# Kernel tuning notes

Measured on AMD Instinct MI355X. Metric: run time of the kernel, lower is better.

The kernel has to match this reference:

```python
import jax, jax.numpy as jnp
import numpy as np

N_NODES = 50000
IN_CH = 128
N_EDGES = 800000
ADD_CONST = 0.5


def setup_inputs() -> dict:
    key = jax.random.key(0)
    k1, k2, k3, k4, k5 = jax.random.split(key, 5)
    x = jax.random.normal(k1, (N_NODES, IN_CH), dtype=jnp.float32)
    edge_index = jax.random.randint(k2, (2, N_EDGES), 0, N_NODES, dtype=jnp.int32)
    edge_weight = jax.random.uniform(k3, (N_EDGES,), dtype=jnp.float32)
    # Linear(2*C -> 1): split into source/target halves (mathematically identical
    # to Linear on concat([x[row], x[col]])). Xavier-uniform-ish scale.
    lim = float(np.sqrt(6.0 / (2 * IN_CH + 1)))
    w_src = jax.random.uniform(k4, (IN_CH,), minval=-lim, maxval=lim, dtype=jnp.float32)
    w_dst = jax.random.uniform(k5, (IN_CH,), minval=-lim, maxval=lim, dtype=jnp.float32)
    b = jnp.zeros((), dtype=jnp.float32)
    return {"x": x, "w_src": w_src, "w_dst": w_dst, "b": b,
            "edge_index": edge_index, "edge_weight": edge_weight}


def _normalize_edge_score(score, row, num_nodes):
    """Per-source-node softmax over strictly-positive scores, +0.5; nodes with
    no positive incident edge keep raw scores (faithful to torch loop)."""
    pos = score > 0
    has_pos = jax.ops.segment_max(pos.astype(jnp.int32), row, num_segments=num_nodes) > 0
    neg_big = jnp.asarray(jnp.finfo(score.dtype).min, score.dtype)
    smax = jax.ops.segment_max(jnp.where(pos, score, neg_big), row, num_segments=num_nodes)
    safe_max = jnp.where(has_pos, smax, 0.0)
    exp_s = jnp.where(pos, jnp.exp(score - safe_max[row]), 0.0)
    denom = jax.ops.segment_sum(exp_s, row, num_segments=num_nodes)
    denom = jnp.where(denom > 0, denom, 1.0)
    soft = jnp.where(pos, exp_s / denom[row] + ADD_CONST, 0.0)
    return jnp.where(has_pos[row], soft, score)


def reference(x, w_src, w_dst, b, edge_index, edge_weight):
    N = x.shape[0]
    row, col = edge_index[0], edge_index[1]

    # Edge score: Linear on concat([x[row], x[col]]) == per-node projections gathered.
    score = (x @ w_src)[row] + (x @ w_dst)[col] + b          # [E]
    norm = _normalize_edge_score(score, row, N)              # [E]

    # Greedy contraction in descending score order. Because the torch loop skips
    # any edge whose endpoint cluster already has size > 1, this is exactly a
    # greedy maximal matching: carry only a per-node 'matched' bitmask.
    perm = jnp.argsort(-norm)
    r_s, c_s, s_s = row[perm], col[perm], norm[perm]

    def step(matched, uv):
        u, v = uv
        ok = (u != v) & ~matched[u] & ~matched[v]
        matched = matched.at[u].set(matched[u] | ok)
        matched = matched.at[v].set(matched[v] | ok)
        return matched, ok

    _, sel = jax.lax.scan(step, jnp.zeros((N,), dtype=bool), (r_s, c_s))  # sel: [E]

    # cluster[v] = u for each selected edge (u, v); everything else identity.
    drop_v = jnp.where(sel, c_s, N)   # out-of-range indices are dropped
    drop_u = jnp.where(sel, r_s, N)
    cluster = jnp.arange(N, dtype=jnp.int32).at[drop_v].set(r_s, mode='drop')
    s_rep = jnp.ones((N,), x.dtype).at[drop_u].set(s_s, mode='drop')       # score of merging edge at rep u
    partner = jnp.arange(N, dtype=jnp.int32).at[drop_u].set(c_s, mode='drop')
    rep_sel = jnp.zeros((N,), bool).at[drop_u].set(True, mode='drop')

    # torch: merged_x[u] = (x[u] + x[v]) * s ; merged_x[v] stays x[v];
    # new_x = index_add by cluster  =>  rep u gets (x[u]+x[v])*s + x[v].
    sum_x = jax.ops.segment_sum(x, cluster, num_segments=N)               # [N, C]
    new_x = sum_x * s_rep[:, None] + jnp.where(rep_sel[:, None], x[partner], 0.0)

    counts = jax.ops.segment_sum(jnp.ones((N,), jnp.int32), cluster, num_segments=N)
    is_rep = counts > 0          # rows of new_x that correspond to surviving clusters

    # Remap edges to cluster representatives; self-loops masked out.
    new_row = cluster[row]
    new_col = cluster[col]
    edge_valid = new_row != new_col

    return new_x, cluster, is_rep, new_row, new_col, edge_valid, edge_weight
```

## Files before the change

### kernel.cpp

```cpp
#include <hip/hip_runtime.h>
#include <cmath>

#define IN_CH 128
#define NBUCK 256
#define LNMAX 196
#define SIDE_BIT (1u << 20)
#define SELF_BIT (1u << 21)
#define PLW(p) __hip_atomic_load((p), __ATOMIC_RELAXED, __HIP_MEMORY_SCOPE_WORKGROUP)

typedef unsigned long long ull;
typedef ull  ull2 __attribute__((ext_vector_type(2)));
typedef float f4  __attribute__((ext_vector_type(4)));

__device__ __forceinline__ ull make_key(float norm, int e) {
    unsigned int b = __float_as_uint(norm);
    unsigned int asc = (b & 0x80000000u) ? ~b : (b | 0x80000000u);
    unsigned int desc = ~asc;
    return (((ull)desc) << 32) | (unsigned int)e;
}

__device__ __forceinline__ float norm_from(float s, unsigned int mb, double den) {
    if (mb != 0u) {
        if (s > 0.0f) {
            float m = __uint_as_float(mb);
            float ev = (float)exp((double)(s - m));
            float d = (float)den;
            return ev / d + 0.5f;
        }
        return 0.0f;
    }
    return s;
}

__global__ void proj_kernel(const float* __restrict__ x, const float* __restrict__ w_src,
                            const float* __restrict__ w_dst, float* __restrict__ p,
                            float* __restrict__ q,
                            ull* __restrict__ wsuit,
                            int* __restrict__ cluster, int* __restrict__ partner,
                            float* __restrict__ s_rep, int* __restrict__ bump,
                            int* __restrict__ btail, int N) {
    int gtid = blockIdx.x * blockDim.x + threadIdx.x;
    if (gtid == 0) *bump = 0;
    if (gtid < NBUCK) btail[gtid] = 0;
    if (gtid < N) {
        wsuit[gtid]    = ~0ULL;
        cluster[gtid]  = gtid;
        partner[gtid]  = gtid;
        s_rep[gtid]    = 1.0f;
    }
    int wave = gtid >> 6;
    int lane = threadIdx.x & 63;
    if (wave >= N) return;
    float2 xv = ((const float2*)(x + (size_t)wave * IN_CH))[lane];
    float2 ws = ((const float2*)w_src)[lane];
    float2 wd = ((const float2*)w_dst)[lane];
    double ap = (double)xv.x * (double)ws.x + (double)xv.y * (double)ws.y;
    double aq = (double)xv.x * (double)wd.x + (double)xv.y * (double)wd.y;
    #pragma unroll
    for (int off = 32; off > 0; off >>= 1) {
        ap += __shfl_down(ap, off);
        aq += __shfl_down(aq, off);
    }
    if (lane == 0) { p[wave] = (float)ap; q[wave] = (float)aq; }
}

__global__ void score_kernel(const int* __restrict__ row, const int* __restrict__ col,
                             const float* __restrict__ p, const float* __restrict__ q,
                             const float* __restrict__ bptr,
                             int2* __restrict__ rc, int* __restrict__ btail,
                             uint2* __restrict__ bucketA, float* __restrict__ bucketS,
                             int bcap, int E) {
    __shared__ int cnt[NBUCK];
    __shared__ int gbase[NBUCK];
    __shared__ int cincl[NBUCK];
    __shared__ unsigned int sA0[2048];
    __shared__ unsigned int sA1[2048];
    __shared__ float sS[2048];
    __shared__ unsigned short sH[2048];
    int t = threadIdx.x;
    int e = blockIdx.x * blockDim.x + t;
    if (t < NBUCK) cnt[t] = 0;
    __syncthreads();
    bool inb = e < E;
    int u = 0, v = 0, l1 = -1, l2 = -1, h1 = 0, h2 = 0;
    float s = 0.0f;
    if (inb) {
        u = row[e]; v = col[e];
        rc[e] = make_int2(u, v);
        s = p[u] + q[v] + bptr[0];
        h1 = u & (NBUCK - 1); l1 = atomicAdd(&cnt[h1], 1);
        if (u != v) {
            h2 = v & (NBUCK - 1); l2 = atomicAdd(&cnt[h2], 1);
        }
    }
    __syncthreads();
    if (t < NBUCK) cincl[t] = cnt[t];
    __syncthreads();
    #pragma unroll
    for (int off = 1; off < NBUCK; off <<= 1) {
        int add = (t < NBUCK && t >= off) ? cincl[t - off] : 0;
        __syncthreads();
        if (t < NBUCK) cincl[t] += add;
        __syncthreads();
    }
    if (t < NBUCK) gbase[t] = atomicAdd(&btail[t], cnt[t]);
    __syncthreads();
    int total = cincl[NBUCK - 1];
    if (l1 >= 0) {
        int idx = cincl[h1] - cnt[h1] + l1;
        sA0[idx] = (unsigned int)e | ((u == v) ? SELF_BIT : 0u);
        sA1[idx] = (unsigned int)v | ((unsigned int)(u >> 8) << 17);
        sS[idx]  = s;
        sH[idx]  = (unsigned short)h1;
    }
    if (l2 >= 0) {
        int idx = cincl[h2] - cnt[h2] + l2;
        sA0[idx] = (unsigned int)e | SIDE_BIT;
        sA1[idx] = (unsigned int)u | ((unsigned int)(v >> 8) << 17);
        sS[idx]  = s;
        sH[idx]  = (unsigned short)h2;
    }
    __syncthreads();
    for (int i = t; i < total; i += blockDim.x) {
        int h = (int)sH[i];
        int pos = gbase[h] + (i - (cincl[h] - cnt[h]));
        size_t g = (size_t)h * bcap + pos;
        bucketA[g] = make_uint2(sA0[i], sA1[i]);
        bucketS[g] = sS[i];
    }
}

__global__ void slot_kernel(uint2* __restrict__ bucketA, const float* __restrict__ bucketS,
                            const int* __restrict__ btail, int bcap,
                            unsigned int* __restrict__ node_max, double* __restrict__ denom,
                            int* __restrict__ bump, int2* __restrict__ seg, int N) {
    __shared__ int hist[LNMAX];
    __shared__ unsigned int maxv[LNMAX];
    __shared__ double dden[LNMAX];
    __shared__ int scan[256];
    __shared__ int basesh;
    int b = blockIdx.x;
    int t = threadIdx.x;
    for (int i = t; i < LNMAX; i += blockDim.x) {
        hist[i] = 0; maxv[i] = 0u; dden[i] = 0.0;
    }
    __syncthreads();
    int n = btail[b];
    uint2* bkA = bucketA + (size_t)b * bcap;
    const float* bkS = bucketS + (size_t)b * bcap;
    for (int i = t; i < n; i += blockDim.x) {
        uint2 en = bkA[i];
        if (!(en.x & SIDE_BIT)) {
            float s = bkS[i];
            if (s > 0.0f) {
                int ln = (int)((en.y >> 17) & 0x1ffu);
                atomicMax(&maxv[ln], __float_as_uint(s));
            }
        }
    }
    __syncthreads();
    for (int i = t; i < n; i += blockDim.x) {
        uint2 en = bkA[i];
        int ln = (int)((en.y >> 17) & 0x1ffu);
        if (!(en.x & SIDE_BIT)) {
            unsigned int mb = maxv[ln];
            float s = bkS[i];
            if (mb != 0u && s > 0.0f) {
                float m = __uint_as_float(mb);
                float ev = (float)exp((double)(s - m));
                atomicAdd(&dden[ln], (double)ev);
            }
        }
        if (en.x & SELF_BIT) {
            bkA[i].x = 0xFFFFFFFFu;
        } else {
            int slot = atomicAdd(&hist[ln], 1);
            bkA[i].x = (en.x & 0x1fffffu) | ((unsigned int)slot << 21);
        }
    }
    __syncthreads();
    if (t < 256) {
        int node = (t << 8) | b;
        int d = (t < LNMAX && node < N) ? hist[t] : 0;
        scan[t] = (d + 3) & ~3;
    }
    __syncthreads();
    #pragma unroll
    for (int off = 1; off < 256; off <<= 1) {
        int add = (t < 256 && t >= off) ? scan[t - off] : 0;
        __syncthreads();
        if (t < 256) scan[t] += add;
        __syncthreads();
    }
    if (t == 255) basesh = atomicAdd(bump, scan[255]);
    __syncthreads();
    if (t < LNMAX) {
        int node = (t << 8) | b;
        if (node < N) {
            int d  = hist[t];
            int pd = (d + 3) & ~3;
            int lo = basesh + scan[t] - pd;
            seg[node]      = make_int2(lo, lo + d);
            node_max[node] = maxv[t];
            denom[node]    = dden[t];
        }
    }
}

__global__ void csr_scatter_kernel(const uint2* __restrict__ bucketA,
                                   const float* __restrict__ bucketS,
                                   const int* __restrict__ btail, int bcap,
                                   const unsigned int* __restrict__ node_max,
                                   const double* __restrict__ denom,
                                   const int2* __restrict__ seg,
                                   ull2* __restrict__ adj, int bpx) {
    int xcd = blockIdx.x & 7;
    int sub = blockIdx.x >> 3;
    for (int bb = 0; bb < NBUCK / 8; ++bb) {
        int b = xcd + (bb << 3);
        int n = btail[b];
        const uint2* bkA = bucketA + (size_t)b * bcap;
        const float* bkS = bucketS + (size_t)b * bcap;
        for (int i = sub * blockDim.x + threadIdx.x; i < n; i += bpx * blockDim.x) {
            uint2 en = bkA[i];
            if (en.x == 0xFFFFFFFFu) continue;
            int e    = (int)(en.x & 0xfffffu);
            int side = (int)((en.x >> 20) & 1u);
            int slot = (int)(en.x >> 21);
            int nb   = (int)(en.y & 0x1ffffu);
            int ln   = (int)((en.y >> 17) & 0x1ffu);
            int dst  = (ln << 8) | b;
            int u    = side ? nb : dst;
            float nv = norm_from(bkS[i], node_max[u], denom[u]);
            ull2 w; w.x = make_key(nv, e); w.y = (ull)nb;
            adj[seg[dst].x + slot] = w;
        }
    }
}

__global__ void suitor_kernel(const int2* __restrict__ seg,
                              const ull2* __restrict__ adj,
                              const int2* __restrict__ rc,
                              ull* __restrict__ ws, int N) {
    int lg   = threadIdx.x >> 5;
    int b    = blockIdx.x;
    int grp  = ((((b >> 3) << 3) + lg) << 3) | (b & 7);
    int lane = threadIdx.x & 31;
    if (grp >= N) return;
    int cur = grp;
    int2 lohi;
    ull excl = 0ULL;
    ull lk = ~0ULL;
    int lv = -1;
    bool reload = true;
    for (int guard = 0; guard < 1000000; ++guard) {
        if (reload) {
            lohi = seg[cur];
            excl = 0ULL;
            lk = ~0ULL; lv = -1;
            for (int i = lohi.x + lane; i < lohi.y; i += 32) {
                ull2 ent = adj[i];
                ull k = ent.x;
                if (k < lk) {
                    int v = (int)ent.y;
                    if (k < PLW(&ws[v])) { lk = k; lv = v; }
                }
            }
            reload = false;
        } else if (lk != ~0ULL && lk <= excl) {
            lk = ~0ULL; lv = -1;
            for (int i = lohi.x + lane; i < lohi.y; i += 32) {
                ull2 ent = adj[i];
                ull k = ent.x;
                if (k > excl && k < lk) {
                    int v = (int)ent.y;
                    if (k < PLW(&ws[v])) { lk = k; lv = v; }
                }
            }
        }
        ull bk = lk; int bv = lv;
        #pragma unroll
        for (int off = 16; off > 0; off >>= 1) {
            ull ok = __shfl_xor(bk, off, 32);
            int ov = __shfl_xor(bv, off, 32);
            if (ok < bk) { bk = ok; bv = ov; }
        }
        if (bk == ~0ULL) break;
        ull old;
        if (lane == 0) old = atomicMin(&ws[bv], bk);
        old = __shfl(old, 0, 32);
        if (old <= bk) {
            excl = bk;
            continue;
        }
        if (old == ~0ULL) break;
        int e = (int)(old & 0xffffffffu);
        int2 pr = rc[e];
        cur = pr.x ^ pr.y ^ bv;
        reload = true;
    }
}

__global__ void extract_kernel(const int2* __restrict__ rc,
                               const float* __restrict__ p, const float* __restrict__ q,
                               const float* __restrict__ bptr,
                               const unsigned int* __restrict__ node_max,
                               const double* __restrict__ denom,
                               const ull* __restrict__ ws,
                               int* __restrict__ cluster, int* __restrict__ partner,
                               float* __restrict__ s_rep, int N) {
    int w = blockIdx.x * blockDim.x + threadIdx.x;
    if (w >= N) return;
    ull k = ws[w];
    if (k == ~0ULL) return;
    int e = (int)(k & 0xffffffffu);
    int2 pr = rc[e];
    int a = pr.x, b = pr.y;
    if (w != a) return;
    if (ws[b] == k) {
        cluster[b] = a;
        partner[a] = b;
        float s = p[a] + q[b] + bptr[0];
        s_rep[a] = norm_from(s, node_max[a], denom[a]);
    }
}

__global__ void out_kernel(const float* __restrict__ x, const int* __restrict__ cluster,
                           const int* __restrict__ partner, const float* __restrict__ s_rep,
                           const int* __restrict__ row, const int* __restrict__ col,
                           const float* __restrict__ w,
                           float* __restrict__ out_newx, float* __restrict__ out_cluster,
                           float* __restrict__ out_isrep, float* __restrict__ out_nrow,
                           float* __restrict__ out_ncol, float* __restrict__ out_valid,
                           float* __restrict__ out_w, int N, int E, int NB1) {
    if ((int)blockIdx.x < NB1) {
        int t = blockIdx.x * blockDim.x + threadIdx.x;
        if (t >= N * (IN_CH / 4)) return;
        int n = t >> 5;
        int c = (t & 31) * 4;
        int cl = cluster[n];
        if ((t & 31) == 0) {
            out_cluster[n] = (float)cl;
            out_isrep[n]   = (cl == n) ? 1.0f : 0.0f;
        }
        f4 o;
        int v = partner[n];
        if (cl != n) {
            o = (f4)0.0f;
        } else if (v != n) {
            float s = s_rep[n];
            f4 xu = *(const f4*)(x + (size_t)n * IN_CH + c);
            f4 xv = *(const f4*)(x + (size_t)v * IN_CH + c);
            o = (xu + xv) * s + xv;
        } else {
            o = *(const f4*)(x + (size_t)n * IN_CH + c);
        }
        __builtin_nontemporal_store(o, (f4*)out_newx + t);
    } else {
        int e = (blockIdx.x - NB1) * blockDim.x + threadIdx.x;
        if (e >= E) return;
        int nr = cluster[row[e]];
        int nc = cluster[col[e]];
        out_nrow[e]  = (float)nr;
        out_ncol[e]  = (float)nc;
        out_valid[e] = (nr != nc) ? 1.0f : 0.0f;
        out_w[e]     = w[e];
    }
}

extern "C" void kernel_launch(void* const* d_in, const int* in_sizes, int n_in_args,
                              void* d_out, int out_size, void* d_ws, size_t ws_size,
                              hipStream_t stream) {
    const float* x     = (const float*)d_in[0];
    const float* w_src = (const float*)d_in[1];
    const float* w_dst = (const float*)d_in[2];
    const float* bptr  = (const float*)d_in[3];
    const int*   ei    = (const int*)d_in[4];
    const float* ew    = (const float*)d_in[5];
    const int N = in_sizes[0] / IN_CH;
    const int E = in_sizes[5];
    const int* row = ei;
    const int* col = ei + E;

    char* wsb = (char*)d_ws;
    size_t off = 0;
    auto alloc = [&](size_t bytes) -> void* {
        off = (off + 255) & ~(size_t)255;
        void* ptr = wsb + off;
        off += bytes;
        return ptr;
    };
    const int bcap = E / 128 + E / 1024 + 1024;
    int2*         rc       = (int2*)alloc((size_t)E * 8);
    ull2*         adj      = (ull2*)alloc(((size_t)2 * E + 4 * N) * 16);
    uint2*        bucketA  = (uint2*)alloc((size_t)NBUCK * bcap * 8);
    float*        bucketS  = (float*)alloc((size_t)NBUCK * bcap * 4);
    unsigned int* node_max = (unsigned int*)alloc((size_t)N * 4);
    double*       denom    = (double*)alloc((size_t)N * 8);
    ull*          wsuit    = (ull*)alloc((size_t)N * 8);
    int2*         seg      = (int2*)alloc((size_t)N * 8);
    int*          cluster  = (int*)alloc((size_t)N * 4);
    int*          partner  = (int*)alloc((size_t)N * 4);
    float*        s_rep    = (float*)alloc((size_t)N * 4);
    float*        pbuf     = (float*)alloc((size_t)N * 4);
    float*        qbuf     = (float*)alloc((size_t)N * 4);
    int*          bump     = (int*)alloc(64);
    int*          btail    = (int*)alloc((size_t)NBUCK * 4);

    float* out       = (float*)d_out;
    float* o_newx    = out;
    float* o_cluster = out + (size_t)N * IN_CH;
    float* o_isrep   = o_cluster + N;
    float* o_nrow    = o_isrep + N;
    float* o_ncol    = o_nrow + E;
    float* o_valid   = o_ncol + E;
    float* o_w       = o_valid + E;

    const int T = 256;
    const int TS = 1024;
    hipLaunchKernelGGL(proj_kernel, dim3((N * 64 + T - 1) / T), dim3(T), 0, stream,
                       x, w_src, w_dst, pbuf, qbuf,
                       wsuit, cluster, partner, s_rep, bump, btail, N);
    hipLaunchKernelGGL(score_kernel, dim3((E + TS - 1) / TS), dim3(TS), 0, stream,
                       row, col, pbuf, qbuf, bptr, rc,
                       btail, bucketA, bucketS, bcap, E);
    hipLaunchKernelGGL(slot_kernel, dim3(NBUCK), dim3(1024), 0, stream,
                       bucketA, bucketS, btail, bcap, node_max, denom, bump, seg, N);
    const int bpx = 80;
    hipLaunchKernelGGL(csr_scatter_kernel, dim3(8 * bpx), dim3(T), 0, stream,
                       bucketA, bucketS, btail, bcap, node_max, denom, seg, adj, bpx);
    const int SB = ((N + 63) / 64) * 8;
    hipLaunchKernelGGL(suitor_kernel, dim3(SB), dim3(T), 0, stream,
                       seg, adj, rc, wsuit, N);
    hipLaunchKernelGGL(extract_kernel, dim3((N + T - 1) / T), dim3(T), 0, stream,
                       rc, pbuf, qbuf, bptr, node_max, denom, wsuit,
                       cluster, partner, s_rep, N);
    const int NB1 = (N * 32 + T - 1) / T;
    const int NB2 = (E + T - 1) / T;
    hipLaunchKernelGGL(out_kernel, dim3(NB1 + NB2), dim3(T), 0, stream,
                       x, cluster, partner, s_rep, row, col, ew,
                       o_newx, o_cluster, o_isrep, o_nrow, o_ncol, o_valid, o_w, N, E, NB1);
    (void)ws_size; (void)out_size; (void)n_in_args;
}
```

Measured before the change: 295.4 us.

## Build per-bucket CSR adjacency in slot kernel and fill keys in place

Per-node counts are now computed and prefix-scanned inside each bucket's block, and edges are written directly into a per-bucket region of the adjacency array. This replaces the global bump allocator and the scattered write from bucket storage into a global CSR. A second pass then converts stored raw scores into sort keys in place, streaming contiguously through the adjacency array. The change drops the write-back of slots to bucket storage and the random adjacency scatter. In exchange the per-bucket segments are no longer padded to multiples of four and the bucket capacity is shrunk, which risks overflow when a bucket is skewed.

```diff
diff --git a/kernel.cpp b/kernel.cpp
--- a/kernel.cpp
+++ b/kernel.cpp
@@ -37,10 +37,9 @@
                             float* __restrict__ q,
                             ull* __restrict__ wsuit,
                             int* __restrict__ cluster, int* __restrict__ partner,
-                            float* __restrict__ s_rep, int* __restrict__ bump,
+                            float* __restrict__ s_rep,
                             int* __restrict__ btail, int N) {
     int gtid = blockIdx.x * blockDim.x + threadIdx.x;
-    if (gtid == 0) *bump = 0;
     if (gtid < NBUCK) btail[gtid] = 0;
     if (gtid < N) {
         wsuit[gtid]    = ~0ULL;
@@ -130,34 +129,50 @@
     }
 }
 
-__global__ void slot_kernel(uint2* __restrict__ bucketA, const float* __restrict__ bucketS,
+__global__ void slot_kernel(const uint2* __restrict__ bucketA,
+                            const float* __restrict__ bucketS,
                             const int* __restrict__ btail, int bcap,
+                            ull2* __restrict__ adj, int* __restrict__ bcount,
                             unsigned int* __restrict__ node_max, double* __restrict__ denom,
-                            int* __restrict__ bump, int2* __restrict__ seg, int N) {
+                            int2* __restrict__ seg, int N) {
     __shared__ int hist[LNMAX];
     __shared__ unsigned int maxv[LNMAX];
     __shared__ double dden[LNMAX];
+    __shared__ int cursor[LNMAX];
     __shared__ int scan[256];
-    __shared__ int basesh;
+    __shared__ int selfcnt;
     int b = blockIdx.x;
     int t = threadIdx.x;
     for (int i = t; i < LNMAX; i += blockDim.x) {
         hist[i] = 0; maxv[i] = 0u; dden[i] = 0.0;
     }
+    if (t == 0) selfcnt = 0;
     __syncthreads();
     int n = btail[b];
-    uint2* bkA = bucketA + (size_t)b * bcap;
+    const uint2* bkA = bucketA + (size_t)b * bcap;
     const float* bkS = bucketS + (size_t)b * bcap;
+    ull2* ad = adj + (size_t)b * bcap;
     for (int i = t; i < n; i += blockDim.x) {
         uint2 en = bkA[i];
+        int ln = (int)((en.y >> 17) & 0x1ffu);
         if (!(en.x & SIDE_BIT)) {
             float s = bkS[i];
-            if (s > 0.0f) {
-                int ln = (int)((en.y >> 17) & 0x1ffu);
-                atomicMax(&maxv[ln], __float_as_uint(s));
-            }
-        }
-    }
+            if (s > 0.0f) atomicMax(&maxv[ln], __float_as_uint(s));
+        }
+        if (en.x & SELF_BIT) atomicAdd(&selfcnt, 1);
+        else                 atomicAdd(&hist[ln], 1);
+    }
+    __syncthreads();
+    if (t < 256) scan[t] = (t < LNMAX) ? hist[t] : 0;
+    __syncthreads();
+    #pragma unroll
+    for (int off = 1; off < 256; off <<= 1) {
+        int add = (t < 256 && t >= off) ? scan[t - off] : 0;
+        __syncthreads();
+        if (t < 256) scan[t] += add;
+        __syncthreads();
+    }
+    if (t < LNMAX) cursor[t] = scan[t] - hist[t];
     __syncthreads();
     for (int i = t; i < n; i += blockDim.x) {
         uint2 en = bkA[i];
@@ -171,35 +186,22 @@
                 atomicAdd(&dden[ln], (double)ev);
             }
         }
-        if (en.x & SELF_BIT) {
-            bkA[i].x = 0xFFFFFFFFu;
-        } else {
-            int slot = atomicAdd(&hist[ln], 1);
-            bkA[i].x = (en.x & 0x1fffffu) | ((unsigned int)slot << 21);
-        }
-    }
-    __syncthreads();
-    if (t < 256) {
-        int node = (t << 8) | b;
-        int d = (t < LNMAX && node < N) ? hist[t] : 0;
-        scan[t] = (d + 3) & ~3;
-    }
-    __syncthreads();
-    #pragma unroll
-    for (int off = 1; off < 256; off <<= 1) {
-        int add = (t < 256 && t >= off) ? scan[t - off] : 0;
-        __syncthreads();
-        if (t < 256) scan[t] += add;
-        __syncthreads();
-    }
-    if (t == 255) basesh = atomicAdd(bump, scan[255]);
-    __syncthreads();
+        if (!(en.x & SELF_BIT)) {
+            int pos = atomicAdd(&cursor[ln], 1);
+            unsigned int meta = (en.x & 0x1fffffu) | ((unsigned int)ln << 21);
+            ull2 w;
+            w.x = ((ull)meta << 32) | (ull)__float_as_uint(bkS[i]);
+            w.y = (ull)(en.y & 0x1ffffu);
+            ad[pos] = w;
+        }
+    }
+    __syncthreads();
+    if (t == 0) bcount[b] = n - selfcnt;
     if (t < LNMAX) {
         int node = (t << 8) | b;
         if (node < N) {
             int d  = hist[t];
-            int pd = (d + 3) & ~3;
-            int lo = basesh + scan[t] - pd;
+            int lo = b * bcap + (scan[t] - d);
             seg[node]      = make_int2(lo, lo + d);
             node_max[node] = maxv[t];
             denom[node]    = dden[t];
@@ -207,33 +209,28 @@
     }
 }
 
-__global__ void csr_scatter_kernel(const uint2* __restrict__ bucketA,
-                                   const float* __restrict__ bucketS,
-                                   const int* __restrict__ btail, int bcap,
-                                   const unsigned int* __restrict__ node_max,
-                                   const double* __restrict__ denom,
-                                   const int2* __restrict__ seg,
-                                   ull2* __restrict__ adj, int bpx) {
+__global__ void key_fill_kernel(ull2* __restrict__ adj,
+                                const int* __restrict__ bcount, int bcap,
+                                const unsigned int* __restrict__ node_max,
+                                const double* __restrict__ denom, int bpx) {
     int xcd = blockIdx.x & 7;
     int sub = blockIdx.x >> 3;
     for (int bb = 0; bb < NBUCK / 8; ++bb) {
         int b = xcd + (bb << 3);
-        int n = btail[b];
-        const uint2* bkA = bucketA + (size_t)b * bcap;
-        const float* bkS = bucketS + (size_t)b * bcap;
+        int n = bcount[b];
+        ull2* ad = adj + (size_t)b * bcap;
         for (int i = sub * blockDim.x + threadIdx.x; i < n; i += bpx * blockDim.x) {
-            uint2 en = bkA[i];
-            if (en.x == 0xFFFFFFFFu) continue;
-            int e    = (int)(en.x & 0xfffffu);
-            int side = (int)((en.x >> 20) & 1u);
-            int slot = (int)(en.x >> 21);
-            int nb   = (int)(en.y & 0x1ffffu);
-            int ln   = (int)((en.y >> 17) & 0x1ffu);
-            int dst  = (ln << 8) | b;
-            int u    = side ? nb : dst;
-            float nv = norm_from(bkS[i], node_max[u], denom[u]);
+            ull2 en = ad[i];
+            unsigned int meta = (unsigned int)(en.x >> 32);
+            float s  = __uint_as_float((unsigned int)(en.x & 0xffffffffu));
+            int e    = (int)(meta & 0xfffffu);
+            int side = (int)((meta >> 20) & 1u);
+            int ln   = (int)(meta >> 21);
+            int nb   = (int)en.y;
+            int u    = side ? nb : ((ln << 8) | b);
+            float nv = norm_from(s, node_max[u], denom[u]);
             ull2 w; w.x = make_key(nv, e); w.y = (ull)nb;
-            adj[seg[dst].x + slot] = w;
+            ad[i] = w;
         }
     }
 }
@@ -390,9 +387,9 @@
         off += bytes;
         return ptr;
     };
-    const int bcap = E / 128 + E / 1024 + 1024;
+    const int bcap = ((E / 128 + 768 + 3) / 4) * 4;
     int2*         rc       = (int2*)alloc((size_t)E * 8);
-    ull2*         adj      = (ull2*)alloc(((size_t)2 * E + 4 * N) * 16);
+    ull2*         adj      = (ull2*)alloc((size_t)NBUCK * bcap * 16);
     uint2*        bucketA  = (uint2*)alloc((size_t)NBUCK * bcap * 8);
     float*        bucketS  = (float*)alloc((size_t)NBUCK * bcap * 4);
     unsigned int* node_max = (unsigned int*)alloc((size_t)N * 4);
@@ -404,8 +401,8 @@
     float*        s_rep    = (float*)alloc((size_t)N * 4);
     float*        pbuf     = (float*)alloc((size_t)N * 4);
     float*        qbuf     = (float*)alloc((size_t)N * 4);
-    int*          bump     = (int*)alloc(64);
     int*          btail    = (int*)alloc((size_t)NBUCK * 4);
+    int*          bcount   = (int*)alloc((size_t)NBUCK * 4);
 
     float* out       = (float*)d_out;
     float* o_newx    = out;
@@ -420,15 +417,16 @@
     const int TS = 1024;
     hipLaunchKernelGGL(proj_kernel, dim3((N * 64 + T - 1) / T), dim3(T), 0, stream,
                        x, w_src, w_dst, pbuf, qbuf,
-                       wsuit, cluster, partner, s_rep, bump, btail, N);
+                       wsuit, cluster, partner, s_rep, btail, N);
     hipLaunchKernelGGL(score_kernel, dim3((E + TS - 1) / TS), dim3(TS), 0, stream,
                        row, col, pbuf, qbuf, bptr, rc,
                        btail, bucketA, bucketS, bcap, E);
     hipLaunchKernelGGL(slot_kernel, dim3(NBUCK), dim3(1024), 0, stream,
-                       bucketA, bucketS, btail, bcap, node_max, denom, bump, seg, N);
+                       bucketA, bucketS, btail, bcap, adj, bcount,
+                       node_max, denom, seg, N);
     const int bpx = 80;
-    hipLaunchKernelGGL(csr_scatter_kernel, dim3(8 * bpx), dim3(T), 0, stream,
-                       bucketA, bucketS, btail, bcap, node_max, denom, seg, adj, bpx);
+    hipLaunchKernelGGL(key_fill_kernel, dim3(8 * bpx), dim3(T), 0, stream,
+                       adj, bcount, bcap, node_max, denom, bpx);
     const int SB = ((N + 63) / 64) * 8;
     hipLaunchKernelGGL(suitor_kernel, dim3(SB), dim3(T), 0, stream,
                        seg, adj, rc, wsuit, N);
```

Measured after the change: 284.9 us (median of 2 runs). 1.04x faster.
